# Performance work log

Measured on AMD Instinct MI355X. Metric: run time of the kernel, lower is better.

## Reference

```python
import jax, jax.numpy as jnp
import numpy as np

S, B, D, H, E, F = 128, 256, 256, 8, 4, 1024
TOPK = 2
HD = D // H


def _ln(x, g, b, eps=1e-5):
    m = x.mean(-1, keepdims=True)
    v = jnp.mean((x - m) ** 2, axis=-1, keepdims=True)
    return (x - m) * jax.lax.rsqrt(v + eps) * g + b


def setup_inputs() -> dict:
    key = jax.random.key(0)
    ks = jax.random.split(key, 12)
    w = lambda k, shape: (jax.random.normal(k, shape, jnp.float32) * 0.05)
    return {
        'x': jax.random.normal(ks[0], (S, B, D), jnp.float32),
        'padding_mask': jnp.zeros((B, S), bool),
        'gate_w': w(ks[1], (D, E)),
        'ln1_g': jnp.ones((E, D), jnp.float32), 'ln1_b': jnp.zeros((E, D), jnp.float32),
        'wq': w(ks[2], (E, D, D)), 'bq': jnp.zeros((E, D), jnp.float32),
        'wk': w(ks[3], (E, D, D)), 'bk': jnp.zeros((E, D), jnp.float32),
        'wv': w(ks[4], (E, D, D)), 'bv': jnp.zeros((E, D), jnp.float32),
        'wo': w(ks[5], (E, D, D)), 'bo': jnp.zeros((E, D), jnp.float32),
        'ln2_g': jnp.ones((E, D), jnp.float32), 'ln2_b': jnp.zeros((E, D), jnp.float32),
        'w1': w(ks[6], (E, D, F)), 'b1': jnp.zeros((E, F), jnp.float32),
        'w2': w(ks[7], (E, F, D)), 'b2': jnp.zeros((E, D), jnp.float32),
    }


def _expert(x, mask_bias, ln1_g, ln1_b, wq, bq, wk, bk, wv, bv, wo, bo,
            ln2_g, ln2_b, w1, b1, w2, b2):
    # x: [S,B,D] sequence-first as in the torch module; one attention expert (Euclidean manifold)
    residual = x
    h = _ln(x, ln1_g, ln1_b)                      # pre_attn_norm
    def heads(t):                                  # [S,B,D] -> [B,H,S,HD]
        return t.reshape(S, B, H, HD).transpose(1, 2, 0, 3)
    q = heads(jnp.einsum('sbd,de->sbe', h, wq) + bq)
    k = heads(jnp.einsum('sbd,de->sbe', h, wk) + bk)
    v = heads(jnp.einsum('sbd,de->sbe', h, wv) + bv)
    scores = jnp.einsum('bhsd,bhtd->bhst', q, k) * (1.0 / np.sqrt(HD)) + mask_bias
    attn = jax.nn.softmax(scores, axis=-1)
    o = jnp.einsum('bhst,bhtd->bhsd', attn, v).transpose(2, 0, 1, 3).reshape(S, B, D)
    o = jnp.einsum('sbd,de->sbe', o, wo) + bo
    x = o + residual
    residual = x
    h = _ln(x, ln2_g, ln2_b)                      # pre_fc_norm
    h = jax.nn.relu(jnp.einsum('sbd,df->sbf', h, w1) + b1)  # fc1 + ReLU
    h = jax.nn.relu(jnp.einsum('sbf,fd->sbd', h, w2) + b2)  # fc2 + ReLU (act in fc2 Sequential)
    return h + residual


def reference(x, padding_mask, gate_w, ln1_g, ln1_b, wq, bq, wk, bk, wv, bv,
              wo, bo, ln2_g, ln2_b, w1, b1, w2, b2):
    mask_bias = jnp.where(padding_mask[:, None, None, :], -1e9, 0.0)  # [B,1,1,S]
    # gate over mean-pooled sequence representation, top-k softmax routing
    logits = x.mean(0) @ gate_w                      # [B,E]
    vals, idx = jax.lax.top_k(logits, TOPK)
    gsm = jax.nn.softmax(vals, axis=-1)
    gates = jnp.zeros_like(logits).at[jnp.arange(B)[:, None], idx].set(gsm)  # [B,E]
    outs = jax.vmap(_expert, in_axes=(None, None) + (0,) * 16)(
        x, mask_bias, ln1_g, ln1_b, wq, bq, wk, bk, wv, bv, wo, bo,
        ln2_g, ln2_b, w1, b1, w2, b2)                # [E,S,B,D]
    return jnp.einsum('esbd,be->sbd', outs, gates)
```

## Files before the change

kernel.cpp:

```cpp
#include <hip/hip_runtime.h>
#include <hip/hip_bf16.h>


#define S_LEN 128
#define BATCH 256
#define DMODEL 256
#define NHEAD 8
#define NEXP 4
#define FDIM 1024
#define HDIM 32
#define MTOKF 65536

typedef unsigned short u16;
typedef __attribute__((ext_vector_type(8))) short short8;
typedef __attribute__((ext_vector_type(4))) float f32x4;
typedef __attribute__((ext_vector_type(4))) unsigned short u16x4;
typedef __attribute__((ext_vector_type(4))) int i32x4;

__device__ __forceinline__ u16 f2bf(float f) {
  union { float f; unsigned u; } c; c.f = f;
  unsigned u = c.u;
  u += 0x7FFFu + ((u >> 16) & 1u);
  return (u16)(u >> 16);
}
__device__ __forceinline__ u16 f2bf_trunc(float f) {
  union { float f; unsigned u; } c; c.f = f;
  return (u16)(c.u >> 16);
}
__device__ __forceinline__ float bf2f(u16 u) {
  union { unsigned u; float f; } c; c.u = ((unsigned)u) << 16;
  return c.f;
}
__device__ __forceinline__ f32x4 mfma16(short8 a, short8 b, f32x4 c) {
  return __builtin_amdgcn_mfma_f32_16x16x32_bf16(a, b, c, 0, 0, 0);
}

__global__ __launch_bounds__(256) void transpose_all(
    const float* __restrict__ wq, const float* __restrict__ wk,
    const float* __restrict__ wv, const float* __restrict__ wo,
    const float* __restrict__ w1, const float* __restrict__ w2,
    u16* __restrict__ wqkvh, u16* __restrict__ woT,
    u16* __restrict__ w1T, u16* __restrict__ w2T) {
  __shared__ float tile[32][33];
  int g = blockIdx.x;
  const float* src; u16* dst; int R, C, es; int e, tx, ty;
  int qkv = 0, base = 0;
  if (g < 1024) {
    int mat = g >> 8, r = g & 255; e = r >> 6; int tl = r & 63; ty = tl >> 3; tx = tl & 7;
    R = 256; C = 256;
    if (mat < 3) { qkv = 1; base = mat * 32; es = 768 * 256; dst = wqkvh;
                   src = (mat == 0) ? wq : (mat == 1) ? wk : wv; }
    else         { src = wo; dst = woT; es = 256 * 256; }
  } else if (g < 2048) {
    int r = g - 1024; e = r >> 8; int tl = r & 255; ty = tl >> 5; tx = tl & 31;
    R = 256; C = 1024; src = w1; dst = w1T; es = 256 * 1024;
  } else {
    int r = g - 2048; e = r >> 8; int tl = r & 255; ty = tl >> 3; tx = tl & 7;
    R = 1024; C = 256; src = w2; dst = w2T; es = 1024 * 256;
  }
  src += (size_t)e * R * C; dst += (size_t)e * es;
  int c0 = tx * 32, r0 = ty * 32;
  int ttx = threadIdx.x & 31, tty = threadIdx.x >> 5;
#pragma unroll
  for (int j = 0; j < 4; ++j)
    tile[tty + j * 8][ttx] = src[(size_t)(r0 + tty + j * 8) * C + c0 + ttx];
  __syncthreads();
#pragma unroll
  for (int j = 0; j < 4; ++j) {
    int cn = c0 + tty + j * 8;
    int drow = qkv ? ((cn >> 5) * 96 + base + (cn & 31)) : cn;
    dst[(size_t)drow * R + r0 + ttx] = f2bf(tile[ttx][tty + j * 8]);
  }
}

__global__ __launch_bounds__(256) void gate_kernel(
    const float* __restrict__ x, const float* __restrict__ gw,
    float* __restrict__ gates) {
  int b = blockIdx.x, d = threadIdx.x;
  float s = 0.f;
  for (int ss = 0; ss < S_LEN; ++ss)
    s += x[((size_t)ss * BATCH + b) * DMODEL + d];
  s *= (1.0f / S_LEN);
  __shared__ float red[256];
  __shared__ float logits_s[NEXP];
  for (int e = 0; e < NEXP; ++e) {
    red[d] = s * gw[d * NEXP + e];
    __syncthreads();
    for (int off = 128; off >= 1; off >>= 1) {
      if (d < off) red[d] += red[d + off];
      __syncthreads();
    }
    if (d == 0) logits_s[e] = red[0];
    __syncthreads();
  }
  if (d == 0) {
    int i1 = 0;
    for (int e = 1; e < NEXP; ++e) if (logits_s[e] > logits_s[i1]) i1 = e;
    int i2 = -1;
    for (int e = 0; e < NEXP; ++e) {
      if (e == i1) continue;
      if (i2 < 0 || logits_s[e] > logits_s[i2]) i2 = e;
    }
    float a = logits_s[i1], c = logits_s[i2];
    float e2 = __expf(c - a);
    float z = 1.0f + e2;
    for (int e = 0; e < NEXP; ++e) gates[b * NEXP + e] = 0.f;
    gates[b * NEXP + i1] = 1.0f / z;
    gates[b * NEXP + i2] = e2 / z;
  }
}

__global__ __launch_bounds__(256) void route_kernel(
    const float* __restrict__ gates, const float* __restrict__ bq,
    const float* __restrict__ bk, const float* __restrict__ bv,
    int* __restrict__ pe, float* __restrict__ pg, float* __restrict__ bqkv) {
  int t = threadIdx.x;
  if (t < BATCH) {
    int c = 0;
    for (int e = 0; e < NEXP; ++e) {
      float gv = gates[t * NEXP + e];
      if (gv > 0.f && c < 2) { pe[2 * t + c] = e; pg[2 * t + c] = gv; ++c; }
    }
  }
  for (int i = t; i < NEXP * 768; i += 256) {
    int e = i / 768, n = i - e * 768;
    int hh = n / 96, off = n - hh * 96;
    float v = (off < 32) ? bq[e * 256 + hh * 32 + off]
            : (off < 64) ? bk[e * 256 + hh * 32 + off - 32]
                         : bv[e * 256 + hh * 32 + off - 64];
    bqkv[i] = v;
  }
}

__global__ __launch_bounds__(256) void ln_kernel(
    const float* __restrict__ X, const float* __restrict__ g,
    const float* __restrict__ bt, const int* __restrict__ pe,
    u16* __restrict__ O) {
  int w = threadIdx.x >> 6, l = threadIdx.x & 63;
  int row = blockIdx.x * 4 + w;
  int d = l * 4;
  int ql = row >> 7;
  int e = pe[ql];
  int s0 = row & 127;
  int b = ql >> 1;
  float4 v = *(const float4*)(X + ((size_t)s0 * BATCH + b) * DMODEL + d);
  float s = v.x + v.y + v.z + v.w;
  float sq = v.x * v.x + v.y * v.y + v.z * v.z + v.w * v.w;
#pragma unroll
  for (int m = 32; m >= 1; m >>= 1) {
    s += __shfl_xor(s, m, 64);
    sq += __shfl_xor(sq, m, 64);
  }
  float mean = s * (1.f / DMODEL);
  float var = sq * (1.f / DMODEL) - mean * mean;
  float inv = rsqrtf(var + 1e-5f);
  const float* ge = g + e * DMODEL;
  const float* be = bt + e * DMODEL;
  u16x4 o;
  o[0] = f2bf((v.x - mean) * inv * ge[d + 0] + be[d + 0]);
  o[1] = f2bf((v.y - mean) * inv * ge[d + 1] + be[d + 1]);
  o[2] = f2bf((v.z - mean) * inv * ge[d + 2] + be[d + 2]);
  o[3] = f2bf((v.w - mean) * inv * ge[d + 3] + be[d + 3]);
  *(u16x4*)&O[(size_t)row * DMODEL + d] = o;
}

__global__ __launch_bounds__(256) void qkvattn(
    const u16* __restrict__ A, const u16* __restrict__ Wh,
    const float* __restrict__ Bh, const int* __restrict__ pe,
    u16* __restrict__ O) {
  __shared__ __align__(16) char smem[29184];
  u16* As = (u16*)smem;
  u16* Bs = (u16*)(smem + 16384);
  u16 (*vT)[136] = (u16(*)[136])smem;
  u16 (*qs)[40]  = (u16(*)[40])(smem + 8704);
  u16 (*ks)[40]  = (u16(*)[40])(smem + 18944);
  u16 (*Ost)[40] = (u16(*)[40])(smem + 8704);
  int t = threadIdx.x, w = t >> 6, l = t & 63;
  u16 (*Pw)[72] = (u16(*)[72])(smem + 8704 + w * 4608);
  int g = blockIdx.x;
  int ql = (g >> 6) * 8 + (g & 7);
  int h = (g >> 3) & 7;
  int e = pe[ql];
  int rowbase = ql * S_LEN;
  const u16* Ab = A + (size_t)rowbase * DMODEL;
  const u16* Bb = Wh + (size_t)(e * 8 + h) * 96 * DMODEL;
  const float* bias = Bh + e * 768 + h * 96;
  int ln15 = l & 15, g4 = l >> 4, xa = l & 7;
  int arow[4], ac[4], brow[3], bc[3];
#pragma unroll
  for (int i = 0; i < 4; ++i) { int sl = t + i * 256; arow[i] = sl >> 3; ac[i] = ((sl & 7) ^ (arow[i] & 7)) * 8; }
#pragma unroll
  for (int i = 0; i < 3; ++i) { int sl = t + i * 256; brow[i] = sl >> 3; bc[i] = ((sl & 7) ^ (brow[i] & 7)) * 8; }
  i32x4 av[4], bv[3];
#pragma unroll
  for (int i = 0; i < 4; ++i) av[i] = *(const i32x4*)&Ab[(size_t)arow[i] * DMODEL + ac[i]];
#pragma unroll
  for (int i = 0; i < 3; ++i) bv[i] = *(const i32x4*)&Bb[(size_t)brow[i] * DMODEL + bc[i]];
  f32x4 acc[2][6] = {};
  for (int k0 = 0; k0 < 256; k0 += 64) {
    __syncthreads();
#pragma unroll
    for (int i = 0; i < 4; ++i) *(i32x4*)&As[(t + i * 256) * 8] = av[i];
#pragma unroll
    for (int i = 0; i < 3; ++i) *(i32x4*)&Bs[(t + i * 256) * 8] = bv[i];
    __syncthreads();
    if (k0 < 192) {
#pragma unroll
      for (int i = 0; i < 4; ++i) av[i] = *(const i32x4*)&Ab[(size_t)arow[i] * DMODEL + k0 + 64 + ac[i]];
#pragma unroll
      for (int i = 0; i < 3; ++i) bv[i] = *(const i32x4*)&Bb[(size_t)brow[i] * DMODEL + k0 + 64 + bc[i]];
    }
#pragma unroll
    for (int kk = 0; kk < 2; ++kk) {
      int ph = (kk * 4 + g4) ^ xa;
      short8 aF[2], bF[6];
#pragma unroll
      for (int i = 0; i < 2; ++i)
        aF[i] = *(const short8*)&As[((w * 32 + i * 16 + ln15) * 8 + ph) * 8];
#pragma unroll
      for (int j = 0; j < 6; ++j)
        bF[j] = *(const short8*)&Bs[((j * 16 + ln15) * 8 + ph) * 8];
#pragma unroll
      for (int i = 0; i < 2; ++i)
#pragma unroll
        for (int j = 0; j < 6; ++j)
          acc[i][j] = mfma16(aF[i], bF[j], acc[i][j]);
    }
  }
  float bb[6];
#pragma unroll
  for (int j = 0; j < 6; ++j) bb[j] = bias[j * 16 + ln15];
  __syncthreads();
#pragma unroll
  for (int i = 0; i < 2; ++i)
#pragma unroll
    for (int j = 0; j < 6; ++j)
#pragma unroll
      for (int r = 0; r < 4; ++r) {
        int m = w * 32 + i * 16 + g4 * 4 + r;
        int c = j * 16 + ln15;
        u16 bf = f2bf(acc[i][j][r] + bb[j]);
        if (c < 32) qs[m][c] = bf;
        else if (c < 64) ks[m][c - 32] = bf;
        else vT[c - 64][m] = bf;
      }
  __syncthreads();
  short8 bQ[2];
#pragma unroll
  for (int j = 0; j < 2; ++j)
    bQ[j] = *(const short8*)&qs[w * 32 + j * 16 + ln15][g4 * 8];
  f32x4 sacc[8][2];
  const f32x4 zero = {0.f, 0.f, 0.f, 0.f};
#pragma unroll
  for (int i = 0; i < 8; ++i) {
    short8 aK = *(const short8*)&ks[i * 16 + ln15][g4 * 8];
#pragma unroll
    for (int j = 0; j < 2; ++j)
      sacc[i][j] = mfma16(aK, bQ[j], zero);
  }
  const float Cc = 0.25505903f;
  float ssum[2];
#pragma unroll
  for (int j = 0; j < 2; ++j) {
    float mx = sacc[0][j][0];
#pragma unroll
    for (int i = 0; i < 8; ++i)
#pragma unroll
      for (int r = 0; r < 4; ++r) mx = fmaxf(mx, sacc[i][j][r]);
    mx = fmaxf(mx, __shfl_xor(mx, 16, 64));
    mx = fmaxf(mx, __shfl_xor(mx, 32, 64));
    float mc = mx * Cc;
    float ss = 0.f;
#pragma unroll
    for (int i = 0; i < 8; ++i)
#pragma unroll
      for (int r = 0; r < 4; ++r) {
        float p = exp2f(fmaf(sacc[i][j][r], Cc, -mc));
        sacc[i][j][r] = p;
        ss += p;
      }
    ss += __shfl_xor(ss, 16, 64);
    ss += __shfl_xor(ss, 32, 64);
    ssum[j] = ss;
  }
  __syncthreads();
  f32x4 oacc[2][2] = {};
#pragma unroll
  for (int hh = 0; hh < 2; ++hh) {
#pragma unroll
    for (int i = 0; i < 4; ++i)
#pragma unroll
      for (int j = 0; j < 2; ++j) {
        u16x4 pk;
#pragma unroll
        for (int r = 0; r < 4; ++r) pk[r] = f2bf_trunc(sacc[4 * hh + i][j][r]);
        *(u16x4*)&Pw[j * 16 + ln15][i * 16 + g4 * 4] = pk;
      }
#pragma unroll
    for (int kk = 0; kk < 2; ++kk) {
      short8 aV[2], bP[2];
#pragma unroll
      for (int i2 = 0; i2 < 2; ++i2)
        aV[i2] = *(const short8*)&vT[i2 * 16 + ln15][hh * 64 + kk * 32 + g4 * 8];
#pragma unroll
      for (int j = 0; j < 2; ++j)
        bP[j] = *(const short8*)&Pw[j * 16 + ln15][kk * 32 + g4 * 8];
#pragma unroll
      for (int i2 = 0; i2 < 2; ++i2)
#pragma unroll
        for (int j = 0; j < 2; ++j)
          oacc[i2][j] = mfma16(aV[i2], bP[j], oacc[i2][j]);
    }
  }
  __syncthreads();
#pragma unroll
  for (int i2 = 0; i2 < 2; ++i2)
#pragma unroll
    for (int j = 0; j < 2; ++j) {
      float inv = 1.0f / ssum[j];
      u16x4 ok;
#pragma unroll
      for (int r = 0; r < 4; ++r) ok[r] = f2bf(oacc[i2][j][r] * inv);
      *(u16x4*)&Ost[w * 32 + j * 16 + ln15][i2 * 16 + g4 * 4] = ok;
    }
  __syncthreads();
  {
    int row = t >> 1;
#pragma unroll
    for (int k = 0; k < 2; ++k) {
      int col = (t & 1) * 16 + k * 8;
      *(int4*)&O[(size_t)(rowbase + row) * DMODEL + h * HDIM + col] =
          *(const int4*)&Ost[row][col];
    }
  }
}

template <int KD, int NT, int EPI, int NB, bool NTA, int GM>
__global__ __launch_bounds__(512) void ggemm(
    const u16* __restrict__ A, const u16* __restrict__ Ball,
    const float* __restrict__ biasAll,
    const int* __restrict__ pe, const float* __restrict__ pg,
    const float* __restrict__ xres, const u16* __restrict__ x1res,
    const float* __restrict__ lng, const float* __restrict__ lnb,
    u16* __restrict__ C, u16* __restrict__ C2, int hb) {
  constexpr int BK = 64;
  __shared__ __align__(16) char smem[49152];
  u16* As = (u16*)smem;
  u16* Bs = (u16*)(smem + 16384);
  u16 (*Cst)[264] = (u16(*)[264])smem;
  int t = threadIdx.x, w = t >> 6, l = t & 63;
  int wr = w >> 2, wc = w & 3;
  int g = blockIdx.x;
  int ql, n0;
  if constexpr (GM == 0) {
    ql = (g / (8 * NB)) * 8 + (g & 7);
    n0 = ((g % (8 * NB)) >> 3) * 256;
  } else if constexpr (GM == 1) {
    int low = g & 15;
    ql = (g & ~15) + ((low & 7) << 1) + (low >> 3);
    n0 = 0;
  } else {
    ql = g; n0 = 0;
  }
  int qg = hb * 256 + ql;
  int e = pe[qg];
  const u16* Ab = A + (size_t)ql * 128 * KD;
  const u16* Bb = Ball + (size_t)e * NT * KD + (size_t)n0 * KD;
  const float* bias = biasAll + e * NT + n0;
  int srow = t >> 3;
  int scol = ((t & 7) ^ (srow & 7)) * 8;
  int xa = l & 7, gq = l >> 4, ln15 = l & 15;
  i32x4 av[2], bv[4];
#pragma unroll
  for (int i = 0; i < 2; ++i) {
    const i32x4* p = (const i32x4*)&Ab[(size_t)(srow + i * 64) * KD + scol];
    av[i] = NTA ? __builtin_nontemporal_load(p) : *p;
  }
#pragma unroll
  for (int k = 0; k < 4; ++k)
    bv[k] = *(const i32x4*)&Bb[(size_t)(srow + k * 64) * KD + scol];
  f32x4 acc[4][4] = {};
  for (int k0 = 0; k0 < KD; k0 += BK) {
    __syncthreads();
#pragma unroll
    for (int i = 0; i < 2; ++i) *(i32x4*)&As[(t + i * 512) * 8] = av[i];
#pragma unroll
    for (int k = 0; k < 4; ++k) *(i32x4*)&Bs[(t + k * 512) * 8] = bv[k];
    __syncthreads();
    if (k0 + BK < KD) {
#pragma unroll
      for (int i = 0; i < 2; ++i) {
        const i32x4* p = (const i32x4*)&Ab[(size_t)(srow + i * 64) * KD + k0 + BK + scol];
        av[i] = NTA ? __builtin_nontemporal_load(p) : *p;
      }
#pragma unroll
      for (int k = 0; k < 4; ++k)
        bv[k] = *(const i32x4*)&Bb[(size_t)(srow + k * 64) * KD + k0 + BK + scol];
    }
#pragma unroll
    for (int kk = 0; kk < 2; ++kk) {
      int colu = ((kk * 4 + gq) ^ xa) * 8;
      short8 aF[4], bF[4];
#pragma unroll
      for (int i = 0; i < 4; ++i)
        aF[i] = *(const short8*)&As[(wr * 64 + i * 16 + ln15) * 64 + colu];
#pragma unroll
      for (int j = 0; j < 4; ++j)
        bF[j] = *(const short8*)&Bs[(wc * 64 + j * 16 + ln15) * 64 + colu];
#pragma unroll
      for (int i = 0; i < 4; ++i)
#pragma unroll
        for (int j = 0; j < 4; ++j)
          acc[i][j] = mfma16(aF[i], bF[j], acc[i][j]);
    }
  }
  int b = qg >> 1;
  float gg = (EPI == 3) ? pg[qg] : 0.f;
  int l4 = (l >> 4) << 2;
  int m0 = ql * 128;
  int prow = t >> 5;
  int pcol = (t & 31) * 8;
#pragma unroll
  for (int half = 0; half < 2; ++half) {
    __syncthreads();
    if (wr == half) {
#pragma unroll
      for (int i = 0; i < 4; ++i)
#pragma unroll
        for (int j = 0; j < 4; ++j) {
          int colb = wc * 64 + j * 16 + ln15;
          float bz = bias[colb];
#pragma unroll
          for (int r = 0; r < 4; ++r) {
            float v = acc[i][j][r] + bz;
            if constexpr (EPI >= 2) v = fmaxf(v, 0.f);
            Cst[i * 16 + l4 + r][colb] = f2bf(v);
          }
        }
    }
    __syncthreads();
#pragma unroll
    for (int p = 0; p < 4; ++p) {
      int rl = p * 16 + prow;
      int m = m0 + half * 64 + rl;
      i32x4 pv = *(const i32x4*)&Cst[rl][pcol];
      size_t idx = (size_t)m * NT + n0 + pcol;
      if constexpr (EPI == 0 || EPI == 2) {
        __builtin_nontemporal_store(pv, (i32x4*)&C[idx]);
      } else if constexpr (EPI == 1) {
        int s = m & 127;
        const float* xr = xres + ((size_t)s * BATCH + b) * DMODEL + pcol;
        const u16* pu = (const u16*)&pv;
        float f0 = bf2f(pu[0]) + xr[0], f1v = bf2f(pu[1]) + xr[1];
        float f2v = bf2f(pu[2]) + xr[2], f3 = bf2f(pu[3]) + xr[3];
        float f4 = bf2f(pu[4]) + xr[4], f5 = bf2f(pu[5]) + xr[5];
        float f6 = bf2f(pu[6]) + xr[6], f7 = bf2f(pu[7]) + xr[7];
        float s1 = f0 + f1v + f2v + f3 + f4 + f5 + f6 + f7;
        float s2 = f0*f0 + f1v*f1v + f2v*f2v + f3*f3 + f4*f4 + f5*f5 + f6*f6 + f7*f7;
#pragma unroll
        for (int mm = 16; mm >= 1; mm >>= 1) {
          s1 += __shfl_xor(s1, mm, 64);
          s2 += __shfl_xor(s2, mm, 64);
        }
        float mean = s1 * (1.f / DMODEL);
        float var = s2 * (1.f / DMODEL) - mean * mean;
        float inv = rsqrtf(var + 1e-5f);
        short8 ox;
        ((u16*)&ox)[0] = f2bf(f0); ((u16*)&ox)[1] = f2bf(f1v);
        ((u16*)&ox)[2] = f2bf(f2v); ((u16*)&ox)[3] = f2bf(f3);
        ((u16*)&ox)[4] = f2bf(f4); ((u16*)&ox)[5] = f2bf(f5);
        ((u16*)&ox)[6] = f2bf(f6); ((u16*)&ox)[7] = f2bf(f7);
        __builtin_nontemporal_store(*(const i32x4*)&ox, (i32x4*)&C[idx]);
        const float* g2 = lng + e * DMODEL + pcol;
        const float* b2p = lnb + e * DMODEL + pcol;
        short8 oh;
        ((u16*)&oh)[0] = f2bf((f0 - mean) * inv * g2[0] + b2p[0]);
        ((u16*)&oh)[1] = f2bf((f1v - mean) * inv * g2[1] + b2p[1]);
        ((u16*)&oh)[2] = f2bf((f2v - mean) * inv * g2[2] + b2p[2]);
        ((u16*)&oh)[3] = f2bf((f3 - mean) * inv * g2[3] + b2p[3]);
        ((u16*)&oh)[4] = f2bf((f4 - mean) * inv * g2[4] + b2p[4]);
        ((u16*)&oh)[5] = f2bf((f5 - mean) * inv * g2[5] + b2p[5]);
        ((u16*)&oh)[6] = f2bf((f6 - mean) * inv * g2[6] + b2p[6]);
        ((u16*)&oh)[7] = f2bf((f7 - mean) * inv * g2[7] + b2p[7]);
        *(short8*)&C2[idx] = oh;
      } else {
        const u16* pu = (const u16*)&pv;
        short8 o;
#pragma unroll
        for (int jj = 0; jj < 8; ++jj)
          ((u16*)&o)[jj] = f2bf(gg * bf2f(pu[jj]));
        *(short8*)&C[idx] = o;
      }
    }
  }
}

__global__ __launch_bounds__(512) void ffn(
    const u16* __restrict__ H2, const u16* __restrict__ W1,
    const float* __restrict__ B1, const u16* __restrict__ W2,
    const float* __restrict__ B2, const u16* __restrict__ X1,
    const int* __restrict__ pe, const float* __restrict__ pg,
    u16* __restrict__ Y) {
  __shared__ __align__(16) char smem[73728];
  u16* As = (u16*)smem;
  u16* Bs = (u16*)(smem + 8192);
  u16* Fc = (u16*)(smem + 40960);
  u16 (*Cst)[264] = (u16(*)[264])smem;
  int t = threadIdx.x, w = t >> 6, l = t & 63;
  int wm = w >> 2, wn = w & 3;
  int ln15 = l & 15, g4 = l >> 4, xa = l & 7;
  int g = blockIdx.x;
  int ql = (g >> 4) * 8 + (g & 7), mh = (g >> 3) & 1;
  int e = pe[ql];
  float gg = pg[ql];
  const u16* Ab = H2 + (size_t)(ql * 128 + mh * 64) * DMODEL;
  const u16* W1e = W1 + (size_t)e * FDIM * DMODEL;
  const u16* W2e = W2 + (size_t)e * DMODEL * FDIM;
  int arow = t >> 3;
  int ac = ((t & 7) ^ (arow & 7)) * 8;
  int brow[4], bc[4];
#pragma unroll
  for (int i = 0; i < 4; ++i) { int sl = t + i * 512; brow[i] = sl >> 3; bc[i] = ((sl & 7) ^ (brow[i] & 7)) * 8; }
  i32x4 av, bv[4];
  av = *(const i32x4*)&Ab[(size_t)arow * DMODEL + ac];
#pragma unroll
  for (int i = 0; i < 4; ++i) bv[i] = *(const i32x4*)&W1e[(size_t)brow[i] * DMODEL + bc[i]];
  f32x4 acc2[2][4] = {};
  for (int fc = 0; fc < 4; ++fc) {
    f32x4 acc1[2][4] = {};
    float b1v[4];
#pragma unroll
    for (int j = 0; j < 4; ++j) b1v[j] = B1[e * FDIM + fc * 256 + wn * 64 + j * 16 + ln15];
#pragma unroll
    for (int s = 0; s < 8; ++s) {
      __syncthreads();
      if (s < 4) *(i32x4*)&As[t * 8] = av;
#pragma unroll
      for (int i = 0; i < 4; ++i) *(i32x4*)&Bs[(t + i * 512) * 8] = bv[i];
      __syncthreads();
      if (s < 3) {
        av = *(const i32x4*)&Ab[(size_t)arow * DMODEL + (s + 1) * 64 + ac];
#pragma unroll
        for (int i = 0; i < 4; ++i)
          bv[i] = *(const i32x4*)&W1e[(size_t)(fc * 256 + brow[i]) * DMODEL + (s + 1) * 64 + bc[i]];
      } else if (s == 3) {
#pragma unroll
        for (int i = 0; i < 4; ++i)
          bv[i] = *(const i32x4*)&W2e[(size_t)brow[i] * FDIM + fc * 256 + bc[i]];
      } else if (s < 7) {
#pragma unroll
        for (int i = 0; i < 4; ++i)
          bv[i] = *(const i32x4*)&W2e[(size_t)brow[i] * FDIM + fc * 256 + (s - 3) * 64 + bc[i]];
      } else if (fc < 3) {
        av = *(const i32x4*)&Ab[(size_t)arow * DMODEL + ac];
#pragma unroll
        for (int i = 0; i < 4; ++i)
          bv[i] = *(const i32x4*)&W1e[(size_t)((fc + 1) * 256 + brow[i]) * DMODEL + bc[i]];
      }
      if (s < 4) {
#pragma unroll
        for (int kk = 0; kk < 2; ++kk) {
          int ph = (kk * 4 + g4) ^ xa;
          short8 aF[2], bF[4];
#pragma unroll
          for (int i = 0; i < 2; ++i)
            aF[i] = *(const short8*)&As[((wm * 32 + i * 16 + ln15) * 8 + ph) * 8];
#pragma unroll
          for (int j = 0; j < 4; ++j)
            bF[j] = *(const short8*)&Bs[((wn * 64 + j * 16 + ln15) * 8 + ph) * 8];
#pragma unroll
          for (int i = 0; i < 2; ++i)
#pragma unroll
            for (int j = 0; j < 4; ++j)
              acc1[i][j] = mfma16(aF[i], bF[j], acc1[i][j]);
        }
        if (s == 3) {
#pragma unroll
          for (int i = 0; i < 2; ++i)
#pragma unroll
            for (int j = 0; j < 4; ++j)
#pragma unroll
              for (int r = 0; r < 4; ++r) {
                int m = wm * 32 + i * 16 + g4 * 4 + r;
                int c = wn * 64 + j * 16 + ln15;
                int cc = c >> 3;
                int ph2 = (cc & 24) | ((cc & 7) ^ (m & 7));
                Fc[(m * 32 + ph2) * 8 + (c & 7)] = f2bf(fmaxf(acc1[i][j][r] + b1v[j], 0.f));
              }
        }
      } else {
        int cb = (s - 4) * 8;
#pragma unroll
        for (int kk = 0; kk < 2; ++kk) {
          int ph = (kk * 4 + g4) ^ xa;
          short8 aF[2], bF[4];
#pragma unroll
          for (int i = 0; i < 2; ++i) {
            int m = wm * 32 + i * 16 + ln15;
            aF[i] = *(const short8*)&Fc[(m * 32 + cb + ph) * 8];
          }
#pragma unroll
          for (int j = 0; j < 4; ++j)
            bF[j] = *(const short8*)&Bs[((wn * 64 + j * 16 + ln15) * 8 + ph) * 8];
#pragma unroll
          for (int i = 0; i < 2; ++i)
#pragma unroll
            for (int j = 0; j < 4; ++j)
              acc2[i][j] = mfma16(aF[i], bF[j], acc2[i][j]);
        }
      }
    }
  }
  __syncthreads();
#pragma unroll
  for (int i = 0; i < 2; ++i)
#pragma unroll
    for (int j = 0; j < 4; ++j) {
      int col = wn * 64 + j * 16 + ln15;
      float bz = B2[e * DMODEL + col];
#pragma unroll
      for (int r = 0; r < 4; ++r)
        Cst[wm * 32 + i * 16 + g4 * 4 + r][col] = f2bf(fmaxf(acc2[i][j][r] + bz, 0.f));
    }
  __syncthreads();
  int prow = t >> 3, pc0 = (t & 7) * 32;
  size_t rbase = (size_t)(ql * 128 + mh * 64 + prow) * DMODEL;
#pragma unroll
  for (int p = 0; p < 4; ++p) {
    int c = pc0 + p * 8;
    i32x4 pv = *(const i32x4*)&Cst[prow][c];
    i32x4 xv4 = __builtin_nontemporal_load((const i32x4*)&X1[rbase + c]);
    const u16* pu = (const u16*)&pv;
    const u16* xv = (const u16*)&xv4;
    short8 o;
#pragma unroll
    for (int jj = 0; jj < 8; ++jj)
      ((u16*)&o)[jj] = f2bf(gg * (bf2f(pu[jj]) + bf2f(xv[jj])));
    *(short8*)&Y[rbase + c] = o;
  }
}

__global__ __launch_bounds__(256) void comb_kernel(
    const u16* __restrict__ y, float* __restrict__ out) {
  int idx = blockIdx.x * 256 + threadIdx.x;
  int n8 = (idx & 31) * 8;
  int b = (idx >> 5) & 255;
  int s = idx >> 13;
  const u16* ra = y + ((size_t)(2 * b) * 128 + s) * DMODEL + n8;
  const u16* rb = ra + 128 * DMODEL;
  short8 a = *(const short8*)ra;
  short8 bb = *(const short8*)rb;
  float* po = out + ((size_t)s * BATCH + b) * DMODEL + n8;
  float4 o0, o1;
  o0.x = bf2f(((u16*)&a)[0]) + bf2f(((u16*)&bb)[0]);
  o0.y = bf2f(((u16*)&a)[1]) + bf2f(((u16*)&bb)[1]);
  o0.z = bf2f(((u16*)&a)[2]) + bf2f(((u16*)&bb)[2]);
  o0.w = bf2f(((u16*)&a)[3]) + bf2f(((u16*)&bb)[3]);
  o1.x = bf2f(((u16*)&a)[4]) + bf2f(((u16*)&bb)[4]);
  o1.y = bf2f(((u16*)&a)[5]) + bf2f(((u16*)&bb)[5]);
  o1.z = bf2f(((u16*)&a)[6]) + bf2f(((u16*)&bb)[6]);
  o1.w = bf2f(((u16*)&a)[7]) + bf2f(((u16*)&bb)[7]);
  *(float4*)po = o0;
  *(float4*)(po + 4) = o1;
}

extern "C" void kernel_launch(void* const* d_in, const int* in_sizes, int n_in,
                              void* d_out, int out_size, void* d_ws, size_t ws_size,
                              hipStream_t stream) {
  const float* x      = (const float*)d_in[0];
  const float* gate_w = (const float*)d_in[2];
  const float* ln1_g  = (const float*)d_in[3];
  const float* ln1_b  = (const float*)d_in[4];
  const float* wq     = (const float*)d_in[5];
  const float* bq     = (const float*)d_in[6];
  const float* wk     = (const float*)d_in[7];
  const float* bk     = (const float*)d_in[8];
  const float* wv     = (const float*)d_in[9];
  const float* bv     = (const float*)d_in[10];
  const float* wo     = (const float*)d_in[11];
  const float* bo     = (const float*)d_in[12];
  const float* ln2_g  = (const float*)d_in[13];
  const float* ln2_b  = (const float*)d_in[14];
  const float* w1     = (const float*)d_in[15];
  const float* b1     = (const float*)d_in[16];
  const float* w2     = (const float*)d_in[17];
  const float* b2     = (const float*)d_in[18];
  float* out = (float*)d_out;

  char* ws = (char*)d_ws;
  int*   pe    = (int*)ws;
  float* pg    = (float*)(ws + 2048);
  float* bqkv  = (float*)(ws + 4096);
  float* gates = (float*)(ws + 16384);
  size_t off = 32768;
  u16* wqkvh = (u16*)(ws + off); off += (size_t)NEXP * 768 * DMODEL * 2;
  u16* woT   = (u16*)(ws + off); off += (size_t)NEXP * DMODEL * DMODEL * 2;
  u16* w1T   = (u16*)(ws + off); off += (size_t)NEXP * FDIM * DMODEL * 2;
  u16* w2T   = (u16*)(ws + off); off += (size_t)NEXP * DMODEL * FDIM * 2;
  char* dyn = ws + off;
  u16* hbuf = (u16*)dyn;
  u16* h2   = hbuf;
  u16* ybuf = hbuf;
  u16* obuf = (u16*)(dyn + (size_t)MTOKF * DMODEL * 2);
  u16* x1   = obuf;

  dim3 blk(256), blk512(512);
  transpose_all<<<dim3(3072), blk, 0, stream>>>(
      wq, wk, wv, wo, w1, w2, wqkvh, woT, w1T, w2T);
  gate_kernel<<<BATCH, blk, 0, stream>>>(x, gate_w, gates);
  route_kernel<<<1, blk, 0, stream>>>(gates, bq, bk, bv, pe, pg, bqkv);

  ln_kernel<<<MTOKF / 4, blk, 0, stream>>>(x, ln1_g, ln1_b, pe, hbuf);
  qkvattn<<<dim3(4096), blk, 0, stream>>>(hbuf, wqkvh, bqkv, pe, obuf);
  ggemm<256, 256, 1, 1, false, 1><<<dim3(512), blk512, 0, stream>>>(
      obuf, woT, bo, pe, pg, x, nullptr, ln2_g, ln2_b, x1, h2, 0);
  ffn<<<dim3(1024), blk512, 0, stream>>>(h2, w1T, b1, w2T, b2, x1, pe, pg, ybuf);
  comb_kernel<<<dim3(4096), blk, 0, stream>>>(ybuf, out);
}
```

Before: 266.8 us.

## Sort FFN blocks by expert and double-buffer global prefetch in ffn kernel

The route kernel now builds a permutation of (batch, slot) pairs grouped by expert, and the ffn kernel reads that permutation so that neighbouring blocks use the same expert weights, which should improve L2 reuse of W1/W2. The ffn loader is changed to prefetch two stages ahead using double-buffered registers, to hide more global-load latency. A launch-bounds occupancy hint of 4 is added. The extra register buffers raise register pressure, and the hint may force spills.

```diff
diff --git a/kernel.cpp b/kernel.cpp
--- a/kernel.cpp
+++ b/kernel.cpp
@@ -113,22 +113,45 @@
 __global__ __launch_bounds__(256) void route_kernel(
     const float* __restrict__ gates, const float* __restrict__ bq,
     const float* __restrict__ bk, const float* __restrict__ bv,
-    int* __restrict__ pe, float* __restrict__ pg, float* __restrict__ bqkv) {
+    int* __restrict__ pe, float* __restrict__ pg, float* __restrict__ bqkv,
+    int* __restrict__ sq) {
+  __shared__ int spe[512];
+  __shared__ int cnt[4], off[4];
   int t = threadIdx.x;
+  if (t < 4) cnt[t] = 0;
   if (t < BATCH) {
     int c = 0;
     for (int e = 0; e < NEXP; ++e) {
       float gv = gates[t * NEXP + e];
-      if (gv > 0.f && c < 2) { pe[2 * t + c] = e; pg[2 * t + c] = gv; ++c; }
+      if (gv > 0.f && c < 2) {
+        pe[2 * t + c] = e; pg[2 * t + c] = gv; spe[2 * t + c] = e; ++c;
+      }
     }
   }
   for (int i = t; i < NEXP * 768; i += 256) {
     int e = i / 768, n = i - e * 768;
-    int hh = n / 96, off = n - hh * 96;
-    float v = (off < 32) ? bq[e * 256 + hh * 32 + off]
-            : (off < 64) ? bk[e * 256 + hh * 32 + off - 32]
-                         : bv[e * 256 + hh * 32 + off - 64];
+    int hh = n / 96, o = n - hh * 96;
+    float v = (o < 32) ? bq[e * 256 + hh * 32 + o]
+            : (o < 64) ? bk[e * 256 + hh * 32 + o - 32]
+                       : bv[e * 256 + hh * 32 + o - 64];
     bqkv[i] = v;
+  }
+  __syncthreads();
+  if (t < BATCH) {
+    atomicAdd(&cnt[spe[2 * t]], 1);
+    atomicAdd(&cnt[spe[2 * t + 1]], 1);
+  }
+  __syncthreads();
+  if (t == 0) {
+    int b0 = 0;
+    for (int e = 0; e < 4; ++e) { off[e] = b0; b0 += cnt[e]; }
+  }
+  __syncthreads();
+  if (t < BATCH) {
+    int p0 = atomicAdd(&off[spe[2 * t]], 1);
+    sq[p0] = 2 * t;
+    int p1 = atomicAdd(&off[spe[2 * t + 1]], 1);
+    sq[p1] = 2 * t + 1;
   }
 }
 
@@ -495,12 +518,12 @@
   }
 }
 
-__global__ __launch_bounds__(512) void ffn(
+__global__ __launch_bounds__(512, 4) void ffn(
     const u16* __restrict__ H2, const u16* __restrict__ W1,
     const float* __restrict__ B1, const u16* __restrict__ W2,
     const float* __restrict__ B2, const u16* __restrict__ X1,
     const int* __restrict__ pe, const float* __restrict__ pg,
-    u16* __restrict__ Y) {
+    const int* __restrict__ sq, u16* __restrict__ Y) {
   __shared__ __align__(16) char smem[73728];
   u16* As = (u16*)smem;
   u16* Bs = (u16*)(smem + 8192);
@@ -510,7 +533,8 @@
   int wm = w >> 2, wn = w & 3;
   int ln15 = l & 15, g4 = l >> 4, xa = l & 7;
   int g = blockIdx.x;
-  int ql = (g >> 4) * 8 + (g & 7), mh = (g >> 3) & 1;
+  int pos = (g >> 4) * 8 + (g & 7), mh = (g >> 3) & 1;
+  int ql = sq[pos];
   int e = pe[ql];
   float gg = pg[ql];
   const u16* Ab = H2 + (size_t)(ql * 128 + mh * 64) * DMODEL;
@@ -521,10 +545,21 @@
   int brow[4], bc[4];
 #pragma unroll
   for (int i = 0; i < 4; ++i) { int sl = t + i * 512; brow[i] = sl >> 3; bc[i] = ((sl & 7) ^ (brow[i] & 7)) * 8; }
-  i32x4 av, bv[4];
-  av = *(const i32x4*)&Ab[(size_t)arow * DMODEL + ac];
-#pragma unroll
-  for (int i = 0; i < 4; ++i) bv[i] = *(const i32x4*)&W1e[(size_t)brow[i] * DMODEL + bc[i]];
+  auto loadB = [&](int u, i32x4* dst) {
+    int fc2 = u >> 3, s2 = u & 7;
+#pragma unroll
+    for (int i = 0; i < 4; ++i) {
+      const u16* p = (s2 < 4)
+        ? &W1e[(size_t)(fc2 * 256 + brow[i]) * DMODEL + s2 * 64 + bc[i]]
+        : &W2e[(size_t)brow[i] * FDIM + fc2 * 256 + (s2 - 4) * 64 + bc[i]];
+      dst[i] = *(const i32x4*)p;
+    }
+  };
+  i32x4 av[2], bv[2][4];
+  av[0] = *(const i32x4*)&Ab[(size_t)arow * DMODEL + ac];
+  loadB(0, bv[0]);
+  av[1] = *(const i32x4*)&Ab[(size_t)arow * DMODEL + 64 + ac];
+  loadB(1, bv[1]);
   f32x4 acc2[2][4] = {};
   for (int fc = 0; fc < 4; ++fc) {
     f32x4 acc1[2][4] = {};
@@ -533,29 +568,19 @@
     for (int j = 0; j < 4; ++j) b1v[j] = B1[e * FDIM + fc * 256 + wn * 64 + j * 16 + ln15];
 #pragma unroll
     for (int s = 0; s < 8; ++s) {
+      int cur = s & 1;
       __syncthreads();
-      if (s < 4) *(i32x4*)&As[t * 8] = av;
-#pragma unroll
-      for (int i = 0; i < 4; ++i) *(i32x4*)&Bs[(t + i * 512) * 8] = bv[i];
+      if (s < 4) *(i32x4*)&As[t * 8] = av[cur];
+#pragma unroll
+      for (int i = 0; i < 4; ++i) *(i32x4*)&Bs[(t + i * 512) * 8] = bv[cur][i];
       __syncthreads();
-      if (s < 3) {
-        av = *(const i32x4*)&Ab[(size_t)arow * DMODEL + (s + 1) * 64 + ac];
-#pragma unroll
-        for (int i = 0; i < 4; ++i)
-          bv[i] = *(const i32x4*)&W1e[(size_t)(fc * 256 + brow[i]) * DMODEL + (s + 1) * 64 + bc[i]];
-      } else if (s == 3) {
-#pragma unroll
-        for (int i = 0; i < 4; ++i)
-          bv[i] = *(const i32x4*)&W2e[(size_t)brow[i] * FDIM + fc * 256 + bc[i]];
-      } else if (s < 7) {
-#pragma unroll
-        for (int i = 0; i < 4; ++i)
-          bv[i] = *(const i32x4*)&W2e[(size_t)brow[i] * FDIM + fc * 256 + (s - 3) * 64 + bc[i]];
-      } else if (fc < 3) {
-        av = *(const i32x4*)&Ab[(size_t)arow * DMODEL + ac];
-#pragma unroll
-        for (int i = 0; i < 4; ++i)
-          bv[i] = *(const i32x4*)&W1e[(size_t)((fc + 1) * 256 + brow[i]) * DMODEL + bc[i]];
+      {
+        int u2 = fc * 8 + s + 2;
+        if (u2 < 32) {
+          int s2 = (s + 2) & 7;
+          if (s2 < 4) av[cur] = *(const i32x4*)&Ab[(size_t)arow * DMODEL + s2 * 64 + ac];
+          loadB(u2, bv[cur]);
+        }
       }
       if (s < 4) {
 #pragma unroll
@@ -692,6 +717,7 @@
   float* pg    = (float*)(ws + 2048);
   float* bqkv  = (float*)(ws + 4096);
   float* gates = (float*)(ws + 16384);
+  int*   sq    = (int*)(ws + 20480);
   size_t off = 32768;
   u16* wqkvh = (u16*)(ws + off); off += (size_t)NEXP * 768 * DMODEL * 2;
   u16* woT   = (u16*)(ws + off); off += (size_t)NEXP * DMODEL * DMODEL * 2;
@@ -708,12 +734,12 @@
   transpose_all<<<dim3(3072), blk, 0, stream>>>(
       wq, wk, wv, wo, w1, w2, wqkvh, woT, w1T, w2T);
   gate_kernel<<<BATCH, blk, 0, stream>>>(x, gate_w, gates);
-  route_kernel<<<1, blk, 0, stream>>>(gates, bq, bk, bv, pe, pg, bqkv);
+  route_kernel<<<1, blk, 0, stream>>>(gates, bq, bk, bv, pe, pg, bqkv, sq);
 
   ln_kernel<<<MTOKF / 4, blk, 0, stream>>>(x, ln1_g, ln1_b, pe, hbuf);
   qkvattn<<<dim3(4096), blk, 0, stream>>>(hbuf, wqkvh, bqkv, pe, obuf);
   ggemm<256, 256, 1, 1, false, 1><<<dim3(512), blk512, 0, stream>>>(
       obuf, woT, bo, pe, pg, x, nullptr, ln2_g, ln2_b, x1, h2, 0);
-  ffn<<<dim3(1024), blk512, 0, stream>>>(h2, w1T, b1, w2T, b2, x1, pe, pg, ybuf);
+  ffn<<<dim3(1024), blk512, 0, stream>>>(h2, w1T, b1, w2T, b2, x1, pe, pg, sq, ybuf);
   comb_kernel<<<dim3(4096), blk, 0, stream>>>(ybuf, out);
 }
```

After: 395.6 us. 48.3% more time.
